# Kernel tuning notes

Hardware: AMD Instinct MI355X
Metric: run time of the kernel (lower is better)

The kernel has to match this reference:

```python
import jax, jax.numpy as jnp
import numpy as np

T, H, F, E, K = 2048, 1024, 1024, 8, 2  # tokens, hidden, ffn, experts, top_k


def setup_inputs() -> dict:
    key = jax.random.key(0)
    k1, k2, k3, k4, k5 = jax.random.split(key, 5)
    hidden_states = jax.random.normal(k1, (T, H), dtype=jnp.float32)
    # router outputs: positive weights (renormalize=False in module, used as-is)
    topk_weights = jax.random.uniform(k2, (T, K), dtype=jnp.float32)
    topk_ids = jax.random.randint(k3, (T, K), 0, E, dtype=jnp.int32)
    # gate_up: (E, 2F, H) with first F rows = gate, last F rows = up
    gate_up_weight = jax.random.normal(k4, (E, 2 * F, H), dtype=jnp.float32) * 0.02
    # down: (E, H, F)
    down_weight = jax.random.normal(k5, (E, H, F), dtype=jnp.float32) * 0.02
    return {
        'hidden_states': hidden_states,
        'topk_weights': topk_weights,
        'topk_ids': topk_ids,
        'gate_up_weight': gate_up_weight,
        'down_weight': down_weight,
    }


def reference(hidden_states, topk_weights, topk_ids, gate_up_weight, down_weight):
    # Fused MoE: per selected expert, y = (silu(x@Wg^T) * (x@Wu^T)) @ Wd^T,
    # combined with router weights (renormalize=False).
    f = down_weight.shape[-1]
    # [T, E, 2F]: gate_up projection for every expert (dense ref for grouped GEMM)
    gu = jnp.einsum('th,eoh->teo', hidden_states, gate_up_weight)
    gate, up = gu[..., :f], gu[..., f:]
    act = jax.nn.silu(gate) * up                     # [T, E, F]
    y = jnp.einsum('tef,ehf->teh', act, down_weight)  # [T, E, H]
    # gather the top-k experts per token and combine
    y_sel = jnp.take_along_axis(y, topk_ids[:, :, None], axis=1)  # [T, K, H]
    out = jnp.sum(y_sel * topk_weights[:, :, None], axis=1)       # [T, H]
    return out.astype(hidden_states.dtype)
```

## Files before the change

### kernel.cpp

```cpp
#include <hip/hip_runtime.h>
#include <hip/hip_bf16.h>

#define T_TOK 2048
#define HID   1024
#define FF    1024
#define NEXP  8
#define NPAIR 4096

#define BM 128
#define BK 32
#define MAX_MT 40
#define MAXROWS (MAX_MT*BM)

using bf16x8 = __attribute__((ext_vector_type(8))) __bf16;
using f32x4  = __attribute__((ext_vector_type(4))) float;

__device__ __forceinline__ unsigned short f2bf(float f) {
    unsigned int u = __float_as_uint(f);
    unsigned int r = (u + 0x7FFF + ((u >> 16) & 1)) >> 16;
    return (unsigned short)r;
}
__device__ __forceinline__ float bf2f(unsigned short s) {
    return __uint_as_float(((unsigned int)s) << 16);
}

__global__ void setup_kernel(const int* __restrict__ ids,
                             const float* __restrict__ tw,
                             int* __restrict__ pair_pos,
                             int* __restrict__ row_tok,
                             float* __restrict__ row_w,
                             int* __restrict__ meta) {
    __shared__ int cnt[NEXP], cnt2[NEXP], base[NEXP];
    int tid = threadIdx.x;
    if (tid < NEXP) { cnt[tid] = 0; cnt2[tid] = 0; }
    __syncthreads();
    for (int p = tid; p < NPAIR; p += 256) atomicAdd(&cnt[ids[p]], 1);
    for (int i = tid; i < MAXROWS; i += 256) row_tok[i] = -1;
    __syncthreads();
    if (tid == 0) {
        int mt = 0;
        for (int e = 0; e < NEXP; e++) {
            meta[e] = mt;
            base[e] = mt * BM;
            mt += (cnt[e] + BM - 1) / BM;
        }
        meta[NEXP] = mt;
    }
    __syncthreads();
    for (int p = tid; p < NPAIR; p += 256) {
        int e = ids[p];
        int pos = base[e] + atomicAdd(&cnt2[e], 1);
        pair_pos[p] = pos;
        row_tok[pos] = p >> 1;
        row_w[pos] = tw[p];
    }
}

#define NB_GU (NEXP*2*FF)
#define NB_DN (NEXP*HID)
__global__ void prep_kernel(const float* __restrict__ wgu,
                            const float* __restrict__ wdn,
                            const float* __restrict__ hs,
                            const int* __restrict__ pair_pos,
                            unsigned short* __restrict__ wgu_b,
                            unsigned short* __restrict__ wdn_b,
                            unsigned short* __restrict__ A) {
    int b = blockIdx.x;
    int c = threadIdx.x * 4;
    const float* src;
    unsigned short* dst;
    if (b < NB_GU) {
        int e = b >> 11;
        int o = b & (2 * FF - 1);
        int nr = (o < FF) ? (2 * o) : (2 * (o - FF) + 1);
        src = wgu + (long)b * HID;
        dst = wgu_b + ((long)e * 2 * FF + nr) * HID;
    } else if (b < NB_GU + NB_DN) {
        int rb = b - NB_GU;
        src = wdn + (long)rb * FF;
        dst = wdn_b + (long)rb * FF;
    } else {
        int p = b - (NB_GU + NB_DN);
        int t = p >> 1;
        src = hs + (long)t * HID;
        dst = A + (long)pair_pos[p] * HID;
    }
    float4 v = *(const float4*)(src + c);
    ushort4 o;
    o.x = f2bf(v.x); o.y = f2bf(v.y); o.z = f2bf(v.z); o.w = f2bf(v.w);
    *(ushort4*)(dst + c) = o;
}

template<int BN_, int EPI>
__global__ __launch_bounds__(256)
void gemm_moe(const unsigned short* __restrict__ A,
              const unsigned short* __restrict__ B,
              unsigned short* __restrict__ Cbf,
              float* __restrict__ outf,
              const int* __restrict__ meta,
              const int* __restrict__ row_tok,
              const float* __restrict__ row_w,
              int K, int Ntot, long Bexp) {
    __shared__ unsigned short As[BM * BK];
    __shared__ unsigned short Bs[BN_ * BK];
    int bx = blockIdx.x, by = blockIdx.y;
    if (bx >= meta[NEXP]) return;
    int e = 0;
#pragma unroll
    for (int i = 1; i < NEXP; i++) if (bx >= meta[i]) e = i;

    long m0 = (long)bx * BM;
    long n0 = (long)by * BN_;
    const unsigned short* Ab = A + m0 * K;
    const unsigned short* Bb = B + (long)e * Bexp + n0 * K;

    int tid = threadIdx.x, lane = tid & 63, wv = tid >> 6;
    const int qr8 = (lane >> 4) * 8;
    const int r = lane & 15;
    const int quad = lane >> 4;
    const int mw = (wv >> 1) * 64, nw = (wv & 1) * (BN_ / 2);
    constexpr int NJ = BN_ / 32;

    f32x4 acc[4][NJ] = {};

    for (int k0 = 0; k0 < K; k0 += BK) {
        __syncthreads();
#pragma unroll
        for (int it = 0; it < 2 + BN_ / 64; it++) {
            int chunk = it * 256 + tid;
            const unsigned short* g;
            unsigned short* l;
            if (it < 2) {
                int row = chunk >> 2, cc = chunk & 3;
                g = Ab + (long)row * K + k0 + cc * 8;
                l = &As[chunk * 8];
            } else {
                int cb = chunk - 512;
                int row = cb >> 2, cc = cb & 3;
                g = Bb + (long)row * K + k0 + cc * 8;
                l = &Bs[cb * 8];
            }
            __builtin_amdgcn_global_load_lds(
                (const __attribute__((address_space(1))) void*)(const void*)g,
                (__attribute__((address_space(3))) void*)(void*)l, 16, 0, 0);
        }
        __syncthreads();

        bf16x8 a[4], b[NJ];
#pragma unroll
        for (int i = 0; i < 4; i++)
            a[i] = *(const bf16x8*)&As[(mw + i * 16 + r) * BK + qr8];
#pragma unroll
        for (int j = 0; j < NJ; j++)
            b[j] = *(const bf16x8*)&Bs[(nw + j * 16 + r) * BK + qr8];
#pragma unroll
        for (int i = 0; i < 4; i++)
#pragma unroll
            for (int j = 0; j < NJ; j++)
                acc[i][j] = __builtin_amdgcn_mfma_f32_16x16x32_bf16(a[i], b[j], acc[i][j], 0, 0, 0);
    }

    if (EPI == 1) {
#pragma unroll
        for (int i = 0; i < 4; i++) {
            long rowb = m0 + mw + i * 16 + quad * 4;
#pragma unroll
            for (int j = 0; j < NJ; j++) {
                int n = (int)n0 + nw + j * 16 + r;
#pragma unroll
                for (int reg = 0; reg < 4; reg++) {
                    float v = acc[i][j][reg];
                    float o = __shfl_xor(v, 1);
                    if (!(r & 1)) {
                        float g = v, u = o;
                        float s = g / (1.f + __expf(-g)) * u;
                        Cbf[(rowb + reg) * (long)(Ntot / 2) + (n >> 1)] = f2bf(s);
                    }
                }
            }
        }
    } else {
#pragma unroll
        for (int i = 0; i < 4; i++) {
            int rowb = (int)m0 + mw + i * 16 + quad * 4;
            int tk[4]; float w[4];
#pragma unroll
            for (int reg = 0; reg < 4; reg++) {
                tk[reg] = row_tok[rowb + reg];
                w[reg] = row_w[rowb + reg];
            }
#pragma unroll
            for (int j = 0; j < NJ; j++) {
                int n = (int)n0 + nw + j * 16 + r;
#pragma unroll
                for (int reg = 0; reg < 4; reg++) {
                    if (tk[reg] >= 0)
                        atomicAdd(outf + (long)tk[reg] * HID + n, w[reg] * acc[i][j][reg]);
                }
            }
        }
    }
}

extern "C" void kernel_launch(void* const* d_in, const int* in_sizes, int n_in,
                              void* d_out, int out_size, void* d_ws, size_t ws_size,
                              hipStream_t stream) {
    const float* hs  = (const float*)d_in[0];
    const float* tw  = (const float*)d_in[1];
    const int*   ids = (const int*)d_in[2];
    const float* wgu = (const float*)d_in[3];
    const float* wdn = (const float*)d_in[4];
    float* out = (float*)d_out;

    char* ws = (char*)d_ws;
    size_t off = 0;
    auto alloc = [&](size_t bytes) -> void* {
        void* p = ws + off;
        off += (bytes + 255) & ~(size_t)255;
        return p;
    };
    unsigned short* wgu_b = (unsigned short*)alloc((size_t)NEXP * 2 * FF * HID * 2);
    unsigned short* wdn_b = (unsigned short*)alloc((size_t)NEXP * HID * FF * 2);
    unsigned short* Abuf  = (unsigned short*)alloc((size_t)MAXROWS * HID * 2);
    unsigned short* act   = (unsigned short*)alloc((size_t)MAXROWS * FF * 2);
    int*   pair_pos = (int*)alloc(NPAIR * 4);
    int*   row_tok  = (int*)alloc(MAXROWS * 4);
    float* row_w    = (float*)alloc(MAXROWS * 4);
    int*   meta     = (int*)alloc(64);

    hipMemsetAsync(Abuf, 0, (size_t)MAXROWS * HID * 2, stream);
    hipMemsetAsync(out, 0, (size_t)T_TOK * HID * 4, stream);

    setup_kernel<<<1, 256, 0, stream>>>(ids, tw, pair_pos, row_tok, row_w, meta);
    prep_kernel<<<NB_GU + NB_DN + NPAIR, 256, 0, stream>>>(
        wgu, wdn, hs, pair_pos, wgu_b, wdn_b, Abuf);

    gemm_moe<64, 1><<<dim3(MAX_MT, (2 * FF) / 64), 256, 0, stream>>>(
        Abuf, wgu_b, act, nullptr, meta, nullptr, nullptr,
        HID, 2 * FF, (long)(2 * FF) * HID);

    gemm_moe<64, 2><<<dim3(MAX_MT, HID / 64), 256, 0, stream>>>(
        act, wdn_b, nullptr, out, meta, row_tok, row_w,
        FF, HID, (long)HID * FF);
}
```

Baseline: 241.1 us.

## Rework MoE setup scan, grid-stride prep, and swizzled double-K-step GEMM tiles

The setup kernel now computes expert offsets with a per-thread count plus shared-memory prefix scan instead of shared atomics, which also makes row placement deterministic. The prep kernel becomes a grid-stride bf16 conversion with a fixed grid, and the gate/up row interleave moves out of it into the GEMM's B-tile address calculation. The GEMM loads two BK slices per barrier pair and XOR-swizzles LDS columns to reduce bank conflicts. Together these aim to cut synchronisation, launch overhead and LDS conflicts, at the cost of more shared memory per block and more complex indexing.

```diff
diff --git a/kernel.cpp b/kernel.cpp
--- a/kernel.cpp
+++ b/kernel.cpp
@@ -8,9 +8,11 @@
 #define NPAIR 4096
 
 #define BM 128
+#define BN 64
 #define BK 32
 #define MAX_MT 40
 #define MAXROWS (MAX_MT*BM)
+#define PPT (NPAIR/256)
 
 using bf16x8 = __attribute__((ext_vector_type(8))) __bf16;
 using f32x4  = __attribute__((ext_vector_type(4))) float;
@@ -20,8 +22,11 @@
     unsigned int r = (u + 0x7FFF + ((u >> 16) & 1)) >> 16;
     return (unsigned short)r;
 }
-__device__ __forceinline__ float bf2f(unsigned short s) {
-    return __uint_as_float(((unsigned int)s) << 16);
+
+__device__ __forceinline__ void gll16(const unsigned short* g, unsigned short* l) {
+    __builtin_amdgcn_global_load_lds(
+        (const __attribute__((address_space(1))) void*)(const void*)g,
+        (__attribute__((address_space(3))) void*)(void*)l, 16, 0, 0);
 }
 
 __global__ void setup_kernel(const int* __restrict__ ids,
@@ -30,34 +35,61 @@
                              int* __restrict__ row_tok,
                              float* __restrict__ row_w,
                              int* __restrict__ meta) {
-    __shared__ int cnt[NEXP], cnt2[NEXP], base[NEXP];
+    __shared__ int S[2][256][NEXP];
+    __shared__ int base[NEXP];
     int tid = threadIdx.x;
-    if (tid < NEXP) { cnt[tid] = 0; cnt2[tid] = 0; }
+    int myc[NEXP];
+    int eloc[PPT];
+#pragma unroll
+    for (int e = 0; e < NEXP; e++) myc[e] = 0;
+#pragma unroll
+    for (int i = 0; i < PPT; i++) {
+        int e = ids[tid * PPT + i];
+        eloc[i] = e;
+#pragma unroll
+        for (int ee = 0; ee < NEXP; ee++) myc[ee] += (e == ee);
+    }
+#pragma unroll
+    for (int e = 0; e < NEXP; e++) S[0][tid][e] = myc[e];
     __syncthreads();
-    for (int p = tid; p < NPAIR; p += 256) atomicAdd(&cnt[ids[p]], 1);
-    for (int i = tid; i < MAXROWS; i += 256) row_tok[i] = -1;
-    __syncthreads();
+    int src = 0;
+    for (int d = 1; d < 256; d <<= 1) {
+#pragma unroll
+        for (int e = 0; e < NEXP; e++) {
+            int v = S[src][tid][e];
+            if (tid >= d) v += S[src][tid - d][e];
+            S[src ^ 1][tid][e] = v;
+        }
+        __syncthreads();
+        src ^= 1;
+    }
     if (tid == 0) {
         int mt = 0;
         for (int e = 0; e < NEXP; e++) {
             meta[e] = mt;
             base[e] = mt * BM;
-            mt += (cnt[e] + BM - 1) / BM;
+            mt += (S[src][255][e] + BM - 1) / BM;
         }
         meta[NEXP] = mt;
     }
+    for (int i = tid; i < MAXROWS; i += 256) row_tok[i] = -1;
     __syncthreads();
-    for (int p = tid; p < NPAIR; p += 256) {
-        int e = ids[p];
-        int pos = base[e] + atomicAdd(&cnt2[e], 1);
+    int off[NEXP];
+#pragma unroll
+    for (int e = 0; e < NEXP; e++) off[e] = base[e] + S[src][tid][e] - myc[e];
+#pragma unroll
+    for (int i = 0; i < PPT; i++) {
+        int p = tid * PPT + i;
+        int e = eloc[i];
+        int pos = 0;
+#pragma unroll
+        for (int ee = 0; ee < NEXP; ee++) if (e == ee) pos = off[ee]++;
         pair_pos[p] = pos;
         row_tok[pos] = p >> 1;
         row_w[pos] = tw[p];
     }
 }
 
-#define NB_GU (NEXP*2*FF)
-#define NB_DN (NEXP*HID)
 __global__ void prep_kernel(const float* __restrict__ wgu,
                             const float* __restrict__ wdn,
                             const float* __restrict__ hs,
@@ -65,33 +97,32 @@
                             unsigned short* __restrict__ wgu_b,
                             unsigned short* __restrict__ wdn_b,
                             unsigned short* __restrict__ A) {
-    int b = blockIdx.x;
-    int c = threadIdx.x * 4;
-    const float* src;
-    unsigned short* dst;
-    if (b < NB_GU) {
-        int e = b >> 11;
-        int o = b & (2 * FF - 1);
-        int nr = (o < FF) ? (2 * o) : (2 * (o - FF) + 1);
-        src = wgu + (long)b * HID;
-        dst = wgu_b + ((long)e * 2 * FF + nr) * HID;
-    } else if (b < NB_GU + NB_DN) {
-        int rb = b - NB_GU;
-        src = wdn + (long)rb * FF;
-        dst = wdn_b + (long)rb * FF;
-    } else {
-        int p = b - (NB_GU + NB_DN);
+    long stride = (long)gridDim.x * blockDim.x;
+    long t0 = (long)blockIdx.x * blockDim.x + threadIdx.x;
+    const long NW1 = (long)NEXP * 2 * FF * HID / 4;
+    for (long i = t0; i < NW1; i += stride) {
+        float4 v = ((const float4*)wgu)[i];
+        ushort4 o; o.x = f2bf(v.x); o.y = f2bf(v.y); o.z = f2bf(v.z); o.w = f2bf(v.w);
+        ((ushort4*)wgu_b)[i] = o;
+    }
+    const long NW2 = (long)NEXP * HID * FF / 4;
+    for (long i = t0; i < NW2; i += stride) {
+        float4 v = ((const float4*)wdn)[i];
+        ushort4 o; o.x = f2bf(v.x); o.y = f2bf(v.y); o.z = f2bf(v.z); o.w = f2bf(v.w);
+        ((ushort4*)wdn_b)[i] = o;
+    }
+    const long NG = (long)NPAIR * HID / 4;
+    for (long i = t0; i < NG; i += stride) {
+        int p = (int)(i >> 8);
+        int c = (int)(i & 255);
         int t = p >> 1;
-        src = hs + (long)t * HID;
-        dst = A + (long)pair_pos[p] * HID;
-    }
-    float4 v = *(const float4*)(src + c);
-    ushort4 o;
-    o.x = f2bf(v.x); o.y = f2bf(v.y); o.z = f2bf(v.z); o.w = f2bf(v.w);
-    *(ushort4*)(dst + c) = o;
-}
-
-template<int BN_, int EPI>
+        float4 v = ((const float4*)(hs + (long)t * HID))[c];
+        ushort4 o; o.x = f2bf(v.x); o.y = f2bf(v.y); o.z = f2bf(v.z); o.w = f2bf(v.w);
+        ((ushort4*)(A + (long)pair_pos[p] * HID))[c] = o;
+    }
+}
+
+template<int EPI>
 __global__ __launch_bounds__(256)
 void gemm_moe(const unsigned short* __restrict__ A,
               const unsigned short* __restrict__ B,
@@ -101,8 +132,8 @@
               const int* __restrict__ row_tok,
               const float* __restrict__ row_w,
               int K, int Ntot, long Bexp) {
-    __shared__ unsigned short As[BM * BK];
-    __shared__ unsigned short Bs[BN_ * BK];
+    __shared__ unsigned short As[2][BM * BK];
+    __shared__ unsigned short Bs[2][BN * BK];
     int bx = blockIdx.x, by = blockIdx.y;
     if (bx >= meta[NEXP]) return;
     int e = 0;
@@ -110,63 +141,65 @@
     for (int i = 1; i < NEXP; i++) if (bx >= meta[i]) e = i;
 
     long m0 = (long)bx * BM;
-    long n0 = (long)by * BN_;
+    int n0 = by * BN;
     const unsigned short* Ab = A + m0 * K;
-    const unsigned short* Bb = B + (long)e * Bexp + n0 * K;
+    const unsigned short* Bb = B + (long)e * Bexp;
 
     int tid = threadIdx.x, lane = tid & 63, wv = tid >> 6;
-    const int qr8 = (lane >> 4) * 8;
     const int r = lane & 15;
-    const int quad = lane >> 4;
-    const int mw = (wv >> 1) * 64, nw = (wv & 1) * (BN_ / 2);
-    constexpr int NJ = BN_ / 32;
-
-    f32x4 acc[4][NJ] = {};
-
-    for (int k0 = 0; k0 < K; k0 += BK) {
+    const int q = lane >> 4;
+    const int mw = (wv >> 1) * 64, nw = (wv & 1) * 32;
+    const int sw = (q ^ ((r >> 1) & 3)) * 8;
+
+    f32x4 acc[4][2] = {};
+
+    for (int k0 = 0; k0 < K; k0 += 2 * BK) {
         __syncthreads();
 #pragma unroll
-        for (int it = 0; it < 2 + BN_ / 64; it++) {
-            int chunk = it * 256 + tid;
-            const unsigned short* g;
-            unsigned short* l;
-            if (it < 2) {
-                int row = chunk >> 2, cc = chunk & 3;
-                g = Ab + (long)row * K + k0 + cc * 8;
-                l = &As[chunk * 8];
-            } else {
-                int cb = chunk - 512;
-                int row = cb >> 2, cc = cb & 3;
-                g = Bb + (long)row * K + k0 + cc * 8;
-                l = &Bs[cb * 8];
-            }
-            __builtin_amdgcn_global_load_lds(
-                (const __attribute__((address_space(1))) void*)(const void*)g,
-                (__attribute__((address_space(3))) void*)(void*)l, 16, 0, 0);
+        for (int s = 0; s < 2; s++) {
+#pragma unroll
+            for (int it = 0; it < 2; it++) {
+                int c = it * 256 + tid;
+                int row = c >> 2, cp = c & 3;
+                int cc = cp ^ ((row >> 1) & 3);
+                gll16(Ab + (long)row * K + (k0 + s * BK + cc * 8), &As[s][c * 8]);
+            }
+            {
+                int c = tid;
+                int row = c >> 2, cp = c & 3;
+                int cc = cp ^ ((row >> 1) & 3);
+                long grow;
+                if (EPI == 1) grow = ((row & 1) ? FF : 0) + ((n0 + row) >> 1);
+                else          grow = n0 + row;
+                gll16(Bb + grow * (long)K + (k0 + s * BK + cc * 8), &Bs[s][c * 8]);
+            }
         }
         __syncthreads();
 
-        bf16x8 a[4], b[NJ];
-#pragma unroll
-        for (int i = 0; i < 4; i++)
-            a[i] = *(const bf16x8*)&As[(mw + i * 16 + r) * BK + qr8];
-#pragma unroll
-        for (int j = 0; j < NJ; j++)
-            b[j] = *(const bf16x8*)&Bs[(nw + j * 16 + r) * BK + qr8];
-#pragma unroll
-        for (int i = 0; i < 4; i++)
-#pragma unroll
-            for (int j = 0; j < NJ; j++)
-                acc[i][j] = __builtin_amdgcn_mfma_f32_16x16x32_bf16(a[i], b[j], acc[i][j], 0, 0, 0);
+#pragma unroll
+        for (int s = 0; s < 2; s++) {
+            bf16x8 a[4], b[2];
+#pragma unroll
+            for (int i = 0; i < 4; i++)
+                a[i] = *(const bf16x8*)&As[s][(mw + i * 16 + r) * BK + sw];
+#pragma unroll
+            for (int j = 0; j < 2; j++)
+                b[j] = *(const bf16x8*)&Bs[s][(nw + j * 16 + r) * BK + sw];
+#pragma unroll
+            for (int i = 0; i < 4; i++)
+#pragma unroll
+                for (int j = 0; j < 2; j++)
+                    acc[i][j] = __builtin_amdgcn_mfma_f32_16x16x32_bf16(a[i], b[j], acc[i][j], 0, 0, 0);
+        }
     }
 
     if (EPI == 1) {
 #pragma unroll
         for (int i = 0; i < 4; i++) {
-            long rowb = m0 + mw + i * 16 + quad * 4;
-#pragma unroll
-            for (int j = 0; j < NJ; j++) {
-                int n = (int)n0 + nw + j * 16 + r;
+            long rowb = m0 + mw + i * 16 + q * 4;
+#pragma unroll
+            for (int j = 0; j < 2; j++) {
+                int n = n0 + nw + j * 16 + r;
 #pragma unroll
                 for (int reg = 0; reg < 4; reg++) {
                     float v = acc[i][j][reg];
@@ -182,7 +215,7 @@
     } else {
 #pragma unroll
         for (int i = 0; i < 4; i++) {
-            int rowb = (int)m0 + mw + i * 16 + quad * 4;
+            int rowb = (int)m0 + mw + i * 16 + q * 4;
             int tk[4]; float w[4];
 #pragma unroll
             for (int reg = 0; reg < 4; reg++) {
@@ -190,8 +223,8 @@
                 w[reg] = row_w[rowb + reg];
             }
 #pragma unroll
-            for (int j = 0; j < NJ; j++) {
-                int n = (int)n0 + nw + j * 16 + r;
+            for (int j = 0; j < 2; j++) {
+                int n = n0 + nw + j * 16 + r;
 #pragma unroll
                 for (int reg = 0; reg < 4; reg++) {
                     if (tk[reg] >= 0)
@@ -232,14 +265,13 @@
     hipMemsetAsync(out, 0, (size_t)T_TOK * HID * 4, stream);
 
     setup_kernel<<<1, 256, 0, stream>>>(ids, tw, pair_pos, row_tok, row_w, meta);
-    prep_kernel<<<NB_GU + NB_DN + NPAIR, 256, 0, stream>>>(
-        wgu, wdn, hs, pair_pos, wgu_b, wdn_b, Abuf);
-
-    gemm_moe<64, 1><<<dim3(MAX_MT, (2 * FF) / 64), 256, 0, stream>>>(
+    prep_kernel<<<2048, 256, 0, stream>>>(wgu, wdn, hs, pair_pos, wgu_b, wdn_b, Abuf);
+
+    gemm_moe<1><<<dim3(MAX_MT, (2 * FF) / BN), 256, 0, stream>>>(
         Abuf, wgu_b, act, nullptr, meta, nullptr, nullptr,
         HID, 2 * FF, (long)(2 * FF) * HID);
 
-    gemm_moe<64, 2><<<dim3(MAX_MT, HID / 64), 256, 0, stream>>>(
+    gemm_moe<2><<<dim3(MAX_MT, HID / BN), 256, 0, stream>>>(
         act, wdn_b, nullptr, out, meta, row_tok, row_w,
         FF, HID, (long)HID * FF);
 }
```

Measured after the change: 237.1 us. About the same (-1.6%).
